# Performance work log

Measured on AMD Instinct MI355X. Metric: run time of the kernel, lower is better.

Reference implementation:

```python
import jax, jax.numpy as jnp
import numpy as np

B, T, M, P = 64, 2048, 512, 512


def setup_inputs() -> dict:
    key = jax.random.key(0)
    ks = jax.random.split(key, 9)
    s = 0.02
    return {
        "hidden_state": jax.random.normal(ks[0], (B, P), jnp.float32),
        "cell_state": jax.random.normal(ks[1], (B, P), jnp.float32),
        "encoder_h": jax.random.normal(ks[2], (B, T, M), jnp.float32),
        # Dense W_d: (2p -> m)
        "W_d": jax.random.normal(ks[3], (2 * P, M), jnp.float32) * s,
        "b_wd": jnp.zeros((M,), jnp.float32),
        # Dense U_d: (m -> m)
        "U_d": jax.random.normal(ks[4], (M, M), jnp.float32) * s,
        "b_ud": jnp.zeros((M,), jnp.float32),
        # Dense v_d: (m -> 1)
        "v_d": jax.random.normal(ks[5], (M, 1), jnp.float32) * s,
        "b_vd": jnp.zeros((1,), jnp.float32),
    }


def reference(hidden_state, cell_state, encoder_h, W_d, b_wd, U_d, b_ud, v_d, b_vd):
    # W_d(RepeatVector(T)(concat([d, s]))): the Dense is applied to the same
    # (B, 2p) vector at every time step, so compute it once and broadcast.
    ds = jnp.concatenate([hidden_state, cell_state], axis=-1)          # (B, 2p)
    ds_proj = ds @ W_d + b_wd                                          # (B, m)
    enc_proj = jnp.einsum('btm,mn->btn', encoder_h, U_d) + b_ud        # (B, T, m)
    e = jnp.tanh(ds_proj[:, None, :] + enc_proj)                       # (B, T, m)
    l = e @ v_d + b_vd                                                 # (B, T, 1)
    return jax.nn.softmax(l, axis=1)                                   # softmax over T
```

## Files before the change

kernel.cpp:

```cpp
#include <hip/hip_runtime.h>
#include <cstdint>
#include <cstddef>

#define ROWS 131072
#define NCOLS 512

typedef float  floatx4 __attribute__((ext_vector_type(4)));
typedef short  shortx8 __attribute__((ext_vector_type(8)));

__device__ __forceinline__ short f2bf_rne(float f) {
  unsigned u = __float_as_uint(f);
  unsigned r = u + 0x7FFFu + ((u >> 16) & 1u);
  return (short)(r >> 16);
}

__device__ __forceinline__ unsigned pack_bf_trunc(float lo, float hi) {
  return __builtin_amdgcn_perm(__float_as_uint(hi), __float_as_uint(lo), 0x07060302u);
}

#define GLOAD_LDS16(gptr, lptr)                                                 \
  __builtin_amdgcn_global_load_lds(                                             \
      (const __attribute__((address_space(1))) void*)(gptr),                    \
      (__attribute__((address_space(3))) void*)(lptr), 16, 0, 0)

extern "C" __global__ __launch_bounds__(256) void prep_kernel(
    const float* __restrict__ hidden, const float* __restrict__ cell,
    const float* __restrict__ W_d, const float* __restrict__ b_wd,
    const float* __restrict__ U_d, const float* __restrict__ b_ud,
    float* __restrict__ S, short* __restrict__ U_T, float* __restrict__ lzero)
{
  int bx = blockIdx.x, tid = threadIdx.x;
  if (bx < 128) {
    int idx = bx * 256 + tid;
    int b = idx >> 9, n = idx & 511;
    const float* h = hidden + b * 512;
    const float* c = cell   + b * 512;
    float acc = b_wd[n] + b_ud[n];
    for (int k = 0; k < 512; ++k) acc = fmaf(h[k], W_d[k * 512 + n], acc);
    for (int k = 0; k < 512; ++k) acc = fmaf(c[k], W_d[(k + 512) * 512 + n], acc);
    S[idx] = acc;
  } else if (bx < 384) {
    int idx = (bx - 128) * 1024 + tid * 4;
    int n = idx >> 9, k0 = idx & 511;
    unsigned lo = (unsigned short)f2bf_rne(U_d[(size_t)(k0 + 0) * 512 + n]) |
                  ((unsigned)(unsigned short)f2bf_rne(U_d[(size_t)(k0 + 1) * 512 + n]) << 16);
    unsigned hi = (unsigned short)f2bf_rne(U_d[(size_t)(k0 + 2) * 512 + n]) |
                  ((unsigned)(unsigned short)f2bf_rne(U_d[(size_t)(k0 + 3) * 512 + n]) << 16);
    uint2 w; w.x = lo; w.y = hi;
    *(uint2*)(U_T + idx) = w;
  } else {
    int idx = ((bx - 384) * 256 + tid) * 4;
    floatx4 z = {0.f, 0.f, 0.f, 0.f};
    *(floatx4*)(lzero + idx) = z;
  }
}

extern "C" __global__ __launch_bounds__(256) void attn_gemm(
    const float* __restrict__ A, const short* __restrict__ UT,
    const float* __restrict__ S, const float* __restrict__ vd,
    float* __restrict__ lout)
{
  __shared__ float Asw[128 * 32];
  __shared__ short Bs[128 * 32];

  const int tid = threadIdx.x;
  const int bx  = blockIdx.x;
  const int xcd = bx & 7;
  const int k7  = bx >> 3;
  const int rb  = xcd * 128 + (k7 >> 2);
  const int cb  = k7 & 3;
  const int row0 = rb * 128;
  const int col0 = cb * 128;
  const int wave = tid >> 6;
  const int lane = tid & 63;
  const int wr = wave >> 1, wc = wave & 1;
  const int q = lane >> 4, l15 = lane & 15;

  const float* asrc[4];
#pragma unroll
  for (int j = 0; j < 4; ++j) {
    int c = wave * 4 + j;
    int m = c * 8 + (lane >> 3);
    int pl = (lane & 7) ^ (m & 7);
    asrc[j] = A + (size_t)(row0 + m) * 512 + pl * 4;
  }
  const short* bsrc[2];
#pragma unroll
  for (int j = 0; j < 2; ++j) {
    int c = wave * 2 + j;
    int n = c * 16 + (lane >> 2);
    int ks = (lane & 3) * 8;
    bsrc[j] = UT + (size_t)(col0 + n) * 512 + ks;
  }

  int aoff0[4], aoff1[4], boff[4];
#pragma unroll
  for (int t = 0; t < 4; ++t) {
    int m = wr * 64 + t * 16 + l15;
    int s = m & 7;
    aoff0[t] = m * 32 + (((2 * q) ^ s) << 2);
    aoff1[t] = m * 32 + ((((2 * q) | 1) ^ s) << 2);
    int n = wc * 64 + t * 16 + l15;
    boff[t] = n * 32 + q * 8;
  }

  floatx4 acc[4][4];
#pragma unroll
  for (int i = 0; i < 4; ++i)
#pragma unroll
    for (int j = 0; j < 4; ++j)
      acc[i][j] = (floatx4){0.f, 0.f, 0.f, 0.f};

  for (int kk = 0; kk < 512; kk += 32) {
    __syncthreads();
#pragma unroll
    for (int j = 0; j < 4; ++j)
      GLOAD_LDS16(asrc[j] + kk, &Asw[(wave * 4 + j) * 256]);
#pragma unroll
    for (int j = 0; j < 2; ++j)
      GLOAD_LDS16(bsrc[j] + kk, &Bs[(wave * 2 + j) * 512]);
    __syncthreads();

    shortx8 af[4], bf[4];
#pragma unroll
    for (int t = 0; t < 4; ++t) {
      floatx4 a0 = *(const floatx4*)(Asw + aoff0[t]);
      floatx4 a1 = *(const floatx4*)(Asw + aoff1[t]);
      union { shortx8 v; unsigned u[4]; } fu;
      fu.u[0] = pack_bf_trunc(a0.x, a0.y);
      fu.u[1] = pack_bf_trunc(a0.z, a0.w);
      fu.u[2] = pack_bf_trunc(a1.x, a1.y);
      fu.u[3] = pack_bf_trunc(a1.z, a1.w);
      af[t] = fu.v;
      bf[t] = *(const shortx8*)(Bs + boff[t]);
    }
#pragma unroll
    for (int tr = 0; tr < 4; ++tr)
#pragma unroll
      for (int tc = 0; tc < 4; ++tc)
        acc[tr][tc] = __builtin_amdgcn_mfma_f32_16x16x32_bf16(
            af[tr], bf[tc], acc[tr][tc], 0, 0, 0);
  }

  const int bb = row0 >> 11;
  const float* Srow = S + bb * 512;
#pragma unroll
  for (int tr = 0; tr < 4; ++tr) {
#pragma unroll
    for (int r = 0; r < 4; ++r) {
      float ssum = 0.f;
#pragma unroll
      for (int tc = 0; tc < 4; ++tc) {
        int n = col0 + wc * 64 + tc * 16 + l15;
        float x = acc[tr][tc][r] + Srow[n];
        x = fminf(15.f, fmaxf(-15.f, x));
        float e2 = __expf(2.f * x);
        float e = (e2 - 1.f) / (e2 + 1.f);
        ssum += e * vd[n];
      }
      ssum += __shfl_xor(ssum, 1);
      ssum += __shfl_xor(ssum, 2);
      ssum += __shfl_xor(ssum, 4);
      ssum += __shfl_xor(ssum, 8);
      if (l15 == 0) {
        int row = row0 + wr * 64 + tr * 16 + q * 4 + r;
        atomicAdd(lout + row, ssum);
      }
    }
  }
}

extern "C" __global__ __launch_bounds__(256) void softmax_t(float* __restrict__ l)
{
  int b = blockIdx.x, tid = threadIdx.x;
  int wave = tid >> 6, lane = tid & 63;
  float* row = l + (size_t)b * 2048;
  float v[8];
  float mx = -3.4e38f;
#pragma unroll
  for (int i = 0; i < 8; ++i) { v[i] = row[tid + i * 256]; mx = fmaxf(mx, v[i]); }
#pragma unroll
  for (int m = 1; m < 64; m <<= 1) mx = fmaxf(mx, __shfl_xor(mx, m));
  __shared__ float red[8];
  if (lane == 0) red[wave] = mx;
  __syncthreads();
  mx = fmaxf(fmaxf(red[0], red[1]), fmaxf(red[2], red[3]));
  float s = 0.f;
#pragma unroll
  for (int i = 0; i < 8; ++i) { v[i] = __expf(v[i] - mx); s += v[i]; }
#pragma unroll
  for (int m = 1; m < 64; m <<= 1) s += __shfl_xor(s, m);
  if (lane == 0) red[4 + wave] = s;
  __syncthreads();
  s = red[4] + red[5] + red[6] + red[7];
  float inv = 1.f / s;
#pragma unroll
  for (int i = 0; i < 8; ++i) row[tid + i * 256] = v[i] * inv;
}

extern "C" void kernel_launch(void* const* d_in, const int* in_sizes, int n_in,
                              void* d_out, int out_size, void* d_ws, size_t ws_size,
                              hipStream_t stream) {
  const float* hidden = (const float*)d_in[0];
  const float* cell   = (const float*)d_in[1];
  const float* enc    = (const float*)d_in[2];
  const float* W_d    = (const float*)d_in[3];
  const float* b_wd   = (const float*)d_in[4];
  const float* U_d    = (const float*)d_in[5];
  const float* b_ud   = (const float*)d_in[6];
  const float* v_d    = (const float*)d_in[7];
  float* out = (float*)d_out;
  float* S   = (float*)d_ws;
  short* UT  = (short*)((char*)d_ws + 32768 * sizeof(float));

  hipLaunchKernelGGL(prep_kernel, dim3(512), dim3(256), 0, stream,
                     hidden, cell, W_d, b_wd, U_d, b_ud, S, UT, out);
  hipLaunchKernelGGL(attn_gemm, dim3(4096), dim3(256), 0, stream,
                     enc, UT, S, v_d, out);
  hipLaunchKernelGGL(softmax_t, dim3(64), dim3(256), 0, stream, out);
}
```

Measured before the change: 531.7 us.

## Pre-convert encoder states to bf16 and use a K=64 bf16 MFMA GEMM

Adds a prep pass that converts the full fp32 encoder tensor to bf16 with round-to-nearest-even into workspace. A new GEMM kernel then loads bf16 A tiles straight into LDS with a K=64 step and an XOR swizzle, which removes the per-iteration fp32-to-bf16 packing and halves the synchronisation count. The U_d transpose now goes through an LDS tile, and the W_d projection uses four accumulators. The cost is an extra full read of the encoder plus a 128MB bf16 write before the GEMM, and the path needs a large workspace; an fp32 fallback keeps the old kernel when the workspace is too small.

After: 549.1 us. +3.3%, slower.

```diff
diff --git a/kernel.cpp b/kernel.cpp
--- a/kernel.cpp
+++ b/kernel.cpp
@@ -2,8 +2,6 @@
 #include <cstdint>
 #include <cstddef>
 
-#define ROWS 131072
-#define NCOLS 512
 
 typedef float  floatx4 __attribute__((ext_vector_type(4)));
 typedef short  shortx8 __attribute__((ext_vector_type(8)));
@@ -13,7 +11,10 @@
   unsigned r = u + 0x7FFFu + ((u >> 16) & 1u);
   return (short)(r >> 16);
 }
-
+__device__ __forceinline__ unsigned pack2_rne(float lo, float hi) {
+  return (unsigned)(unsigned short)f2bf_rne(lo) |
+         ((unsigned)(unsigned short)f2bf_rne(hi) << 16);
+}
 __device__ __forceinline__ unsigned pack_bf_trunc(float lo, float hi) {
   return __builtin_amdgcn_perm(__float_as_uint(hi), __float_as_uint(lo), 0x07060302u);
 }
@@ -27,41 +28,70 @@
     const float* __restrict__ hidden, const float* __restrict__ cell,
     const float* __restrict__ W_d, const float* __restrict__ b_wd,
     const float* __restrict__ U_d, const float* __restrict__ b_ud,
-    float* __restrict__ S, short* __restrict__ U_T, float* __restrict__ lzero)
+    const float* __restrict__ enc,
+    float* __restrict__ S, short* __restrict__ UT, short* __restrict__ Abf,
+    float* __restrict__ lzero)
 {
-  int bx = blockIdx.x, tid = threadIdx.x;
-  if (bx < 128) {
+  __shared__ short Ls[64 * 65];
+  const int bx = blockIdx.x, tid = threadIdx.x;
+  if (bx >= 320) {
+    size_t i0 = (size_t)(bx - 320) * 2048 + (size_t)tid * 8;
+    floatx4 a = *(const floatx4*)(enc + i0);
+    floatx4 b = *(const floatx4*)(enc + i0 + 4);
+    union { shortx8 s; unsigned u[4]; } o;
+    o.u[0] = pack2_rne(a.x, a.y);
+    o.u[1] = pack2_rne(a.z, a.w);
+    o.u[2] = pack2_rne(b.x, b.y);
+    o.u[3] = pack2_rne(b.z, b.w);
+    *(shortx8*)(Abf + i0) = o.s;
+  } else if (bx < 128) {
     int idx = bx * 256 + tid;
     int b = idx >> 9, n = idx & 511;
     const float* h = hidden + b * 512;
     const float* c = cell   + b * 512;
-    float acc = b_wd[n] + b_ud[n];
-    for (int k = 0; k < 512; ++k) acc = fmaf(h[k], W_d[k * 512 + n], acc);
-    for (int k = 0; k < 512; ++k) acc = fmaf(c[k], W_d[(k + 512) * 512 + n], acc);
-    S[idx] = acc;
-  } else if (bx < 384) {
-    int idx = (bx - 128) * 1024 + tid * 4;
-    int n = idx >> 9, k0 = idx & 511;
-    unsigned lo = (unsigned short)f2bf_rne(U_d[(size_t)(k0 + 0) * 512 + n]) |
-                  ((unsigned)(unsigned short)f2bf_rne(U_d[(size_t)(k0 + 1) * 512 + n]) << 16);
-    unsigned hi = (unsigned short)f2bf_rne(U_d[(size_t)(k0 + 2) * 512 + n]) |
-                  ((unsigned)(unsigned short)f2bf_rne(U_d[(size_t)(k0 + 3) * 512 + n]) << 16);
-    uint2 w; w.x = lo; w.y = hi;
-    *(uint2*)(U_T + idx) = w;
+    float a0 = b_wd[n] + b_ud[n], a1 = 0.f, a2 = 0.f, a3 = 0.f;
+    for (int k = 0; k < 512; k += 4) {
+      a0 = fmaf(h[k + 0], W_d[(k + 0) * 512 + n], a0);
+      a1 = fmaf(h[k + 1], W_d[(k + 1) * 512 + n], a1);
+      a2 = fmaf(h[k + 2], W_d[(k + 2) * 512 + n], a2);
+      a3 = fmaf(h[k + 3], W_d[(k + 3) * 512 + n], a3);
+    }
+    for (int k = 0; k < 512; k += 4) {
+      a0 = fmaf(c[k + 0], W_d[(512 + k + 0) * 512 + n], a0);
+      a1 = fmaf(c[k + 1], W_d[(512 + k + 1) * 512 + n], a1);
+      a2 = fmaf(c[k + 2], W_d[(512 + k + 2) * 512 + n], a2);
+      a3 = fmaf(c[k + 3], W_d[(512 + k + 3) * 512 + n], a3);
+    }
+    S[idx] = (a0 + a1) + (a2 + a3);
+  } else if (bx < 192) {
+    int bt = bx - 128;
+    int k0 = (bt >> 3) * 64, n0 = (bt & 7) * 64;
+#pragma unroll
+    for (int it = 0; it < 16; ++it) {
+      int e = it * 256 + tid;
+      int r = e >> 6, c = e & 63;
+      Ls[r * 65 + c] = f2bf_rne(U_d[(size_t)(k0 + r) * 512 + n0 + c]);
+    }
+    __syncthreads();
+#pragma unroll
+    for (int it = 0; it < 16; ++it) {
+      int e = it * 256 + tid;
+      int rn = e >> 6, ck = e & 63;
+      UT[(size_t)(n0 + rn) * 512 + k0 + ck] = Ls[ck * 65 + rn];
+    }
   } else {
-    int idx = ((bx - 384) * 256 + tid) * 4;
-    floatx4 z = {0.f, 0.f, 0.f, 0.f};
-    *(floatx4*)(lzero + idx) = z;
-  }
-}
-
-extern "C" __global__ __launch_bounds__(256) void attn_gemm(
-    const float* __restrict__ A, const short* __restrict__ UT,
+    int idx = ((bx - 192) * 256 + tid) * 4;
+    *(floatx4*)(lzero + idx) = (floatx4){0.f, 0.f, 0.f, 0.f};
+  }
+}
+
+extern "C" __global__ __launch_bounds__(256, 4) void attn_gemm_bf(
+    const short* __restrict__ A, const short* __restrict__ UT,
     const float* __restrict__ S, const float* __restrict__ vd,
     float* __restrict__ lout)
 {
-  __shared__ float Asw[128 * 32];
-  __shared__ short Bs[128 * 32];
+  __shared__ short As[128 * 64];
+  __shared__ short Bs[128 * 64];
 
   const int tid = threadIdx.x;
   const int bx  = blockIdx.x;
@@ -76,6 +106,114 @@
   const int wr = wave >> 1, wc = wave & 1;
   const int q = lane >> 4, l15 = lane & 15;
 
+  int aoffg[4], boffg[4];
+#pragma unroll
+  for (int j = 0; j < 4; ++j) {
+    int c = j * 64 + lane;
+    int r = c >> 3, p = c & 7;
+    int m = wave * 32 + r;
+    int l = p ^ (m & 7);
+    aoffg[j] = (row0 + m) * 512 + l * 8;
+    boffg[j] = (col0 + m) * 512 + l * 8;
+  }
+
+  const int arow = (wr * 64 + l15) * 64;
+  const int brow = (wc * 64 + l15) * 64;
+  const int s7 = l15 & 7;
+  const int abase0 = arow + ((q) ^ s7) * 8;
+  const int abase1 = arow + ((4 + q) ^ s7) * 8;
+  const int bbase0 = brow + ((q) ^ s7) * 8;
+  const int bbase1 = brow + ((4 + q) ^ s7) * 8;
+
+  floatx4 acc[4][4];
+#pragma unroll
+  for (int i = 0; i < 4; ++i)
+#pragma unroll
+    for (int j = 0; j < 4; ++j)
+      acc[i][j] = (floatx4){0.f, 0.f, 0.f, 0.f};
+
+  for (int kk = 0; kk < 512; kk += 64) {
+    __syncthreads();
+#pragma unroll
+    for (int j = 0; j < 4; ++j)
+      GLOAD_LDS16(A + aoffg[j] + kk, &As[wave * 2048 + j * 512]);
+#pragma unroll
+    for (int j = 0; j < 4; ++j)
+      GLOAD_LDS16(UT + boffg[j] + kk, &Bs[wave * 2048 + j * 512]);
+    __syncthreads();
+
+    shortx8 af[4], bf[4];
+#pragma unroll
+    for (int t = 0; t < 4; ++t) {
+      af[t] = *(const shortx8*)(As + abase0 + t * 1024);
+      bf[t] = *(const shortx8*)(Bs + bbase0 + t * 1024);
+    }
+#pragma unroll
+    for (int tr = 0; tr < 4; ++tr)
+#pragma unroll
+      for (int tc = 0; tc < 4; ++tc)
+        acc[tr][tc] = __builtin_amdgcn_mfma_f32_16x16x32_bf16(
+            af[tr], bf[tc], acc[tr][tc], 0, 0, 0);
+#pragma unroll
+    for (int t = 0; t < 4; ++t) {
+      af[t] = *(const shortx8*)(As + abase1 + t * 1024);
+      bf[t] = *(const shortx8*)(Bs + bbase1 + t * 1024);
+    }
+#pragma unroll
+    for (int tr = 0; tr < 4; ++tr)
+#pragma unroll
+      for (int tc = 0; tc < 4; ++tc)
+        acc[tr][tc] = __builtin_amdgcn_mfma_f32_16x16x32_bf16(
+            af[tr], bf[tc], acc[tr][tc], 0, 0, 0);
+  }
+
+  const float* Srow = S + (row0 >> 11) * 512;
+#pragma unroll
+  for (int tr = 0; tr < 4; ++tr) {
+#pragma unroll
+    for (int r = 0; r < 4; ++r) {
+      float ssum = 0.f;
+#pragma unroll
+      for (int tc = 0; tc < 4; ++tc) {
+        int n = col0 + wc * 64 + tc * 16 + l15;
+        float x = acc[tr][tc][r] + Srow[n];
+        x = fminf(15.f, fmaxf(-15.f, x));
+        float e2 = __expf(2.f * x);
+        ssum += ((e2 - 1.f) / (e2 + 1.f)) * vd[n];
+      }
+      ssum += __shfl_xor(ssum, 1);
+      ssum += __shfl_xor(ssum, 2);
+      ssum += __shfl_xor(ssum, 4);
+      ssum += __shfl_xor(ssum, 8);
+      if (l15 == 0) {
+        int row = row0 + wr * 64 + tr * 16 + q * 4 + r;
+        atomicAdd(lout + row, ssum);
+      }
+    }
+  }
+}
+
+extern "C" __global__ __launch_bounds__(256) void attn_gemm_f32(
+    const float* __restrict__ A, const short* __restrict__ UT,
+    const float* __restrict__ S, const float* __restrict__ vd,
+    float* __restrict__ lout)
+{
+  __shared__ float Asw[128 * 32];
+  __shared__ short Bs[128 * 32];
+
+  const int tid = threadIdx.x;
+  const int bx  = blockIdx.x;
+  const int xcd = bx & 7;
+  const int k7  = bx >> 3;
+  const int rb  = xcd * 128 + (k7 >> 2);
+  const int cb  = k7 & 3;
+  const int row0 = rb * 128;
+  const int col0 = cb * 128;
+  const int wave = tid >> 6;
+  const int lane = tid & 63;
+  const int wr = wave >> 1, wc = wave & 1;
+  const int q = lane >> 4, l15 = lane & 15;
+
   const float* asrc[4];
 #pragma unroll
   for (int j = 0; j < 4; ++j) {
@@ -142,8 +280,7 @@
             af[tr], bf[tc], acc[tr][tc], 0, 0, 0);
   }
 
-  const int bb = row0 >> 11;
-  const float* Srow = S + bb * 512;
+  const float* Srow = S + (row0 >> 11) * 512;
 #pragma unroll
   for (int tr = 0; tr < 4; ++tr) {
 #pragma unroll
@@ -155,8 +292,7 @@
         float x = acc[tr][tc][r] + Srow[n];
         x = fminf(15.f, fmaxf(-15.f, x));
         float e2 = __expf(2.f * x);
-        float e = (e2 - 1.f) / (e2 + 1.f);
-        ssum += e * vd[n];
+        ssum += ((e2 - 1.f) / (e2 + 1.f)) * vd[n];
       }
       ssum += __shfl_xor(ssum, 1);
       ssum += __shfl_xor(ssum, 2);
@@ -211,11 +347,20 @@
   const float* v_d    = (const float*)d_in[7];
   float* out = (float*)d_out;
   float* S   = (float*)d_ws;
-  short* UT  = (short*)((char*)d_ws + 32768 * sizeof(float));
-
-  hipLaunchKernelGGL(prep_kernel, dim3(512), dim3(256), 0, stream,
-                     hidden, cell, W_d, b_wd, U_d, b_ud, S, UT, out);
-  hipLaunchKernelGGL(attn_gemm, dim3(4096), dim3(256), 0, stream,
-                     enc, UT, S, v_d, out);
+  short* UT  = (short*)((char*)d_ws + 131072);
+  short* Abf = (short*)((char*)d_ws + 131072 + 524288);
+
+  const size_t need = 131072ull + 524288ull + 134217728ull;
+  if (ws_size >= need) {
+    hipLaunchKernelGGL(prep_kernel, dim3(320 + 32768), dim3(256), 0, stream,
+                       hidden, cell, W_d, b_wd, U_d, b_ud, enc, S, UT, Abf, out);
+    hipLaunchKernelGGL(attn_gemm_bf, dim3(4096), dim3(256), 0, stream,
+                       Abf, UT, S, v_d, out);
+  } else {
+    hipLaunchKernelGGL(prep_kernel, dim3(320), dim3(256), 0, stream,
+                       hidden, cell, W_d, b_wd, U_d, b_ud, enc, S, UT, Abf, out);
+    hipLaunchKernelGGL(attn_gemm_f32, dim3(4096), dim3(256), 0, stream,
+                       enc, UT, S, v_d, out);
+  }
   hipLaunchKernelGGL(softmax_t, dim3(64), dim3(256), 0, stream, out);
 }
```
